# Optimization experiments

Measured on AMD Instinct MI355X. Metric: run time of the kernel, lower is better.

The kernel has to match this reference:

```python
import jax, jax.numpy as jnp
import numpy as np

N = 65536      # flattened latent vectors (e.g. 64 images x 32x32 latents)
K = 1024       # num_embeddings (codebook size)
D = 64         # latent_dim


def setup_inputs() -> dict:
    key = jax.random.key(0)
    k_x, k_e = jax.random.split(key)
    inputs = jax.random.normal(k_x, (N, D), dtype=jnp.float32)
    # codebook initialized ~ tf.random_normal_initializer (stddev=0.05)
    embeddings = jax.random.normal(k_e, (K, D), dtype=jnp.float32) * 0.05
    return {"inputs": inputs, "embeddings": embeddings}


def reference(inputs, embeddings):
    # Pairwise L2 distances ||x_n - e_k||_2 -> [N, K].
    x_sq = jnp.sum(inputs * inputs, axis=-1, keepdims=True)        # [N, 1]
    e_sq = jnp.sum(embeddings * embeddings, axis=-1)               # [K]
    cross = inputs @ embeddings.T                                   # [N, K]
    sq_dist = x_sq + e_sq[None, :] - 2.0 * cross                    # [N, K]
    return jnp.sqrt(jnp.maximum(sq_dist, 0.0))
```

## Files before the change

kernel.cpp:

```cpp
#include <hip/hip_runtime.h>


typedef __attribute__((ext_vector_type(8))) short short8;
typedef __attribute__((ext_vector_type(4))) float floatx4;

typedef __attribute__((address_space(3))) unsigned int lds_u32;
typedef __attribute__((address_space(1))) const unsigned int glb_u32;

#define LSTR 72
#define N_ROWS 65536
#define K_ROWS 1024

#define WS_XB  0u
#define WS_EB  9437184u
#define WS_XSQ 9584640u
#define WS_ESQ 9846784u

__device__ __forceinline__ unsigned short f2bf(float f) {
    unsigned int u = __float_as_uint(f);
    u += 0x7FFFu + ((u >> 16) & 1u);
    return (unsigned short)(u >> 16);
}
__device__ __forceinline__ float bf2f(unsigned short h) {
    return __uint_as_float(((unsigned int)h) << 16);
}

__global__ __launch_bounds__(256) void vq_prep(const float* __restrict__ X,
                                               const float* __restrict__ E,
                                               unsigned short* __restrict__ Xb,
                                               unsigned short* __restrict__ Eb,
                                               float* __restrict__ xsq,
                                               float* __restrict__ esq) {
    const int t = blockIdx.x * 256 + threadIdx.x;
    const int row = t >> 3;
    const int c8 = (t & 7) * 8;
    const float* src;
    unsigned short* dst;
    float* sq;
    int r;
    if (row < N_ROWS) {
        r = row;
        src = X + (size_t)r * 64 + c8;
        dst = Xb + (size_t)r * LSTR + c8;
        sq = xsq;
    } else {
        r = row - N_ROWS;
        src = E + (size_t)r * 64 + c8;
        dst = Eb + (size_t)r * LSTR + c8;
        sq = esq;
    }
    float4 v0 = *(const float4*)src;
    float4 v1 = *(const float4*)(src + 4);
    unsigned short h[8] = {f2bf(v0.x), f2bf(v0.y), f2bf(v0.z), f2bf(v0.w),
                           f2bf(v1.x), f2bf(v1.y), f2bf(v1.z), f2bf(v1.w)};
    float s = 0.f;
    short8 pk;
    #pragma unroll
    for (int j = 0; j < 8; ++j) {
        float f = bf2f(h[j]);
        s = fmaf(f, f, s);
        pk[j] = (short)h[j];
    }
    *(short8*)dst = pk;
    s += __shfl_down(s, 4, 8);
    s += __shfl_down(s, 2, 8);
    s += __shfl_down(s, 1, 8);
    if ((t & 7) == 0) sq[r] = s;
}

__global__ __launch_bounds__(256) void vq_main(const unsigned short* __restrict__ Xb,
                                               const unsigned short* __restrict__ Eb,
                                               const float* __restrict__ xsq,
                                               const float* __restrict__ esq,
                                               float* __restrict__ out,
                                               int Ktot) {
    __shared__ unsigned short lds[2 * 128 * LSTR];
    __shared__ float s_xsq[128];
    __shared__ float s_esq[128];

    const int tid = threadIdx.x;
    const int w = tid >> 6;
    const int lane = tid & 63;
    const size_t m0 = (size_t)blockIdx.y * 128;
    const int n0 = blockIdx.x * 128;

    const char* srcA = (const char*)(Xb + m0 * LSTR);
    const char* srcB = (const char*)(Eb + (size_t)n0 * LSTR);
    #pragma unroll
    for (int c = 0; c < 9; ++c) {
        const int chunk = w * 9 + c;
        const int off = chunk * 1024 + lane * 16;
        const char* g = (chunk < 18) ? (srcA + off) : (srcB + (off - 18432));
        __builtin_amdgcn_global_load_lds((glb_u32*)g,
                                         (lds_u32*)((char*)lds + chunk * 1024),
                                         16, 0, 0);
    }
    if (tid < 128) s_xsq[tid] = xsq[m0 + tid];
    else           s_esq[tid - 128] = esq[n0 + tid - 128];
    __syncthreads();

    const unsigned short* lA = lds;
    const unsigned short* lB = lds + 128 * LSTR;

    const int quad = lane >> 4;
    const int l16 = lane & 15;
    const int wm = (w >> 1) * 64;
    const int wn = (w & 1) * 64;

    short8 a0[4], a1[4], b0[4], b1[4];
    #pragma unroll
    for (int t = 0; t < 4; ++t) {
        const int ar = wm + t * 16 + l16;
        a0[t] = *(const short8*)&lA[ar * LSTR + quad * 8];
        a1[t] = *(const short8*)&lA[ar * LSTR + 32 + quad * 8];
        const int br = wn + t * 16 + l16;
        b0[t] = *(const short8*)&lB[br * LSTR + quad * 8];
        b1[t] = *(const short8*)&lB[br * LSTR + 32 + quad * 8];
    }

    floatx4 acc[4][4];
    #pragma unroll
    for (int i = 0; i < 4; ++i)
        #pragma unroll
        for (int j = 0; j < 4; ++j)
            acc[i][j] = (floatx4){0.f, 0.f, 0.f, 0.f};

    #pragma unroll
    for (int i = 0; i < 4; ++i)
        #pragma unroll
        for (int j = 0; j < 4; ++j) {
            acc[i][j] = __builtin_amdgcn_mfma_f32_16x16x32_bf16(a0[i], b0[j], acc[i][j], 0, 0, 0);
            acc[i][j] = __builtin_amdgcn_mfma_f32_16x16x32_bf16(a1[i], b1[j], acc[i][j], 0, 0, 0);
        }

    #pragma unroll
    for (int i = 0; i < 4; ++i) {
        const int mrow = wm + i * 16 + quad * 4;
        float xq[4];
        #pragma unroll
        for (int r = 0; r < 4; ++r) xq[r] = s_xsq[mrow + r];
        #pragma unroll
        for (int j = 0; j < 4; ++j) {
            const int ncol = wn + j * 16 + l16;
            const float eq = s_esq[ncol];
            float* op = out + (m0 + mrow) * Ktot + (n0 + ncol);
            #pragma unroll
            for (int r = 0; r < 4; ++r) {
                float d = xq[r] + eq - 2.0f * acc[i][j][r];
                d = fmaxf(d, 0.0f);
                __builtin_nontemporal_store(sqrtf(d), op + (size_t)r * Ktot);
            }
        }
    }
}

extern "C" void kernel_launch(void* const* d_in, const int* in_sizes, int n_in,
                              void* d_out, int out_size, void* d_ws, size_t ws_size,
                              hipStream_t stream) {
    const float* X = (const float*)d_in[0];
    const float* E = (const float*)d_in[1];
    float* out = (float*)d_out;
    const int K = in_sizes[1] / 64;

    char* ws = (char*)d_ws;
    unsigned short* Xb = (unsigned short*)(ws + WS_XB);
    unsigned short* Eb = (unsigned short*)(ws + WS_EB);
    float* xsq = (float*)(ws + WS_XSQ);
    float* esq = (float*)(ws + WS_ESQ);

    vq_prep<<<dim3((N_ROWS + K_ROWS) * 8 / 256), dim3(256), 0, stream>>>(X, E, Xb, Eb, xsq, esq);

    dim3 grid(K / 128, N_ROWS / 128);
    vq_main<<<grid, dim3(256), 0, stream>>>(Xb, Eb, xsq, esq, out, K);
}
```

Measured before the change: 312.0 us.

## Fuse bf16 conversion prep into distance kernel and swizzle tile order

Removes the separate prep kernel that converted X and E to bf16 and computed squared norms through a workspace. Each block now loads its fp32 X and E tiles directly, converts them to bf16 in registers, writes them to LDS and computes the norms locally. This drops one kernel launch and the workspace round trip. In exchange, each X tile is converted 8 times (once per codebook tile) and E is reconverted by every block. A 1D grid with a block-index swizzle is also introduced, which changes the tile traversal order for cache locality.

```diff
diff --git a/kernel.cpp b/kernel.cpp
--- a/kernel.cpp
+++ b/kernel.cpp
@@ -4,17 +4,8 @@
 typedef __attribute__((ext_vector_type(8))) short short8;
 typedef __attribute__((ext_vector_type(4))) float floatx4;
 
-typedef __attribute__((address_space(3))) unsigned int lds_u32;
-typedef __attribute__((address_space(1))) const unsigned int glb_u32;
-
 #define LSTR 72
 #define N_ROWS 65536
-#define K_ROWS 1024
-
-#define WS_XB  0u
-#define WS_EB  9437184u
-#define WS_XSQ 9584640u
-#define WS_ESQ 9846784u
 
 __device__ __forceinline__ unsigned short f2bf(float f) {
     unsigned int u = __float_as_uint(f);
@@ -25,83 +16,73 @@
     return __uint_as_float(((unsigned int)h) << 16);
 }
 
-__global__ __launch_bounds__(256) void vq_prep(const float* __restrict__ X,
-                                               const float* __restrict__ E,
-                                               unsigned short* __restrict__ Xb,
-                                               unsigned short* __restrict__ Eb,
-                                               float* __restrict__ xsq,
-                                               float* __restrict__ esq) {
-    const int t = blockIdx.x * 256 + threadIdx.x;
-    const int row = t >> 3;
-    const int c8 = (t & 7) * 8;
-    const float* src;
-    unsigned short* dst;
-    float* sq;
-    int r;
-    if (row < N_ROWS) {
-        r = row;
-        src = X + (size_t)r * 64 + c8;
-        dst = Xb + (size_t)r * LSTR + c8;
-        sq = xsq;
-    } else {
-        r = row - N_ROWS;
-        src = E + (size_t)r * 64 + c8;
-        dst = Eb + (size_t)r * LSTR + c8;
-        sq = esq;
-    }
-    float4 v0 = *(const float4*)src;
-    float4 v1 = *(const float4*)(src + 4);
-    unsigned short h[8] = {f2bf(v0.x), f2bf(v0.y), f2bf(v0.z), f2bf(v0.w),
-                           f2bf(v1.x), f2bf(v1.y), f2bf(v1.z), f2bf(v1.w)};
-    float s = 0.f;
-    short8 pk;
-    #pragma unroll
-    for (int j = 0; j < 8; ++j) {
-        float f = bf2f(h[j]);
-        s = fmaf(f, f, s);
-        pk[j] = (short)h[j];
-    }
-    *(short8*)dst = pk;
-    s += __shfl_down(s, 4, 8);
-    s += __shfl_down(s, 2, 8);
-    s += __shfl_down(s, 1, 8);
-    if ((t & 7) == 0) sq[r] = s;
-}
-
-__global__ __launch_bounds__(256) void vq_main(const unsigned short* __restrict__ Xb,
-                                               const unsigned short* __restrict__ Eb,
-                                               const float* __restrict__ xsq,
-                                               const float* __restrict__ esq,
-                                               float* __restrict__ out,
-                                               int Ktot) {
+__global__ __launch_bounds__(256) void vq_fused(const float* __restrict__ X,
+                                                const float* __restrict__ E,
+                                                float* __restrict__ out,
+                                                int Ktot) {
     __shared__ unsigned short lds[2 * 128 * LSTR];
     __shared__ float s_xsq[128];
     __shared__ float s_esq[128];
 
     const int tid = threadIdx.x;
+
+    const int nxb = Ktot >> 7;
+    const int cpx = gridDim.x >> 3;
+    const int bid = blockIdx.x;
+    const int swz = (bid & 7) * cpx + (bid >> 3);
+    const int bx = swz % nxb;
+    const int by = swz / nxb;
+    const size_t m0 = (size_t)by * 128;
+    const int n0 = bx * 128;
+
+    unsigned short* ldsA = lds;
+    unsigned short* ldsB = lds + 128 * LSTR;
+
+    const float* gX = X + m0 * 64;
+    const float* gE = E + (size_t)n0 * 64;
+
+    float4 v[8][2];
+    #pragma unroll
+    for (int it = 0; it < 4; ++it) {
+        const int g = it * 256 + tid;
+        const int row = g >> 3, c8 = (g & 7) * 8;
+        const float* p = gX + row * 64 + c8;
+        v[it][0] = *(const float4*)p;
+        v[it][1] = *(const float4*)(p + 4);
+        const float* q = gE + row * 64 + c8;
+        v[4 + it][0] = *(const float4*)q;
+        v[4 + it][1] = *(const float4*)(q + 4);
+    }
+
+    #pragma unroll
+    for (int half = 0; half < 2; ++half) {
+        unsigned short* dst = half ? ldsB : ldsA;
+        float* sq = half ? s_esq : s_xsq;
+        #pragma unroll
+        for (int it = 0; it < 4; ++it) {
+            const int g = it * 256 + tid;
+            const int row = g >> 3, c8 = (g & 7) * 8;
+            const float* f = (const float*)&v[half * 4 + it][0];
+            float s = 0.f;
+            short8 pk;
+            #pragma unroll
+            for (int j = 0; j < 8; ++j) {
+                const unsigned short h = f2bf(f[j]);
+                const float r = bf2f(h);
+                s = fmaf(r, r, s);
+                pk[j] = (short)h;
+            }
+            *(short8*)&dst[row * LSTR + c8] = pk;
+            s += __shfl_down(s, 4, 8);
+            s += __shfl_down(s, 2, 8);
+            s += __shfl_down(s, 1, 8);
+            if ((tid & 7) == 0) sq[row] = s;
+        }
+    }
+    __syncthreads();
+
     const int w = tid >> 6;
     const int lane = tid & 63;
-    const size_t m0 = (size_t)blockIdx.y * 128;
-    const int n0 = blockIdx.x * 128;
-
-    const char* srcA = (const char*)(Xb + m0 * LSTR);
-    const char* srcB = (const char*)(Eb + (size_t)n0 * LSTR);
-    #pragma unroll
-    for (int c = 0; c < 9; ++c) {
-        const int chunk = w * 9 + c;
-        const int off = chunk * 1024 + lane * 16;
-        const char* g = (chunk < 18) ? (srcA + off) : (srcB + (off - 18432));
-        __builtin_amdgcn_global_load_lds((glb_u32*)g,
-                                         (lds_u32*)((char*)lds + chunk * 1024),
-                                         16, 0, 0);
-    }
-    if (tid < 128) s_xsq[tid] = xsq[m0 + tid];
-    else           s_esq[tid - 128] = esq[n0 + tid - 128];
-    __syncthreads();
-
-    const unsigned short* lA = lds;
-    const unsigned short* lB = lds + 128 * LSTR;
-
     const int quad = lane >> 4;
     const int l16 = lane & 15;
     const int wm = (w >> 1) * 64;
@@ -111,11 +92,11 @@
     #pragma unroll
     for (int t = 0; t < 4; ++t) {
         const int ar = wm + t * 16 + l16;
-        a0[t] = *(const short8*)&lA[ar * LSTR + quad * 8];
-        a1[t] = *(const short8*)&lA[ar * LSTR + 32 + quad * 8];
+        a0[t] = *(const short8*)&ldsA[ar * LSTR + quad * 8];
+        a1[t] = *(const short8*)&ldsA[ar * LSTR + 32 + quad * 8];
         const int br = wn + t * 16 + l16;
-        b0[t] = *(const short8*)&lB[br * LSTR + quad * 8];
-        b1[t] = *(const short8*)&lB[br * LSTR + 32 + quad * 8];
+        b0[t] = *(const short8*)&ldsB[br * LSTR + quad * 8];
+        b1[t] = *(const short8*)&ldsB[br * LSTR + 32 + quad * 8];
     }
 
     floatx4 acc[4][4];
@@ -162,14 +143,6 @@
     float* out = (float*)d_out;
     const int K = in_sizes[1] / 64;
 
-    char* ws = (char*)d_ws;
-    unsigned short* Xb = (unsigned short*)(ws + WS_XB);
-    unsigned short* Eb = (unsigned short*)(ws + WS_EB);
-    float* xsq = (float*)(ws + WS_XSQ);
-    float* esq = (float*)(ws + WS_ESQ);
-
-    vq_prep<<<dim3((N_ROWS + K_ROWS) * 8 / 256), dim3(256), 0, stream>>>(X, E, Xb, Eb, xsq, esq);
-
-    dim3 grid(K / 128, N_ROWS / 128);
-    vq_main<<<grid, dim3(256), 0, stream>>>(Xb, Eb, xsq, esq, out, K);
+    const int tiles = (N_ROWS / 128) * (K / 128);
+    vq_fused<<<dim3(tiles), dim3(256), 0, stream>>>(X, E, out, K);
 }
```

Result: no change. 315.9 us (+1.2%).
